# Optimization experiments

Hardware: AMD Instinct MI355X
Metric: run time of the kernel (lower is better)

## Reference

```python
import jax, jax.numpy as jnp
import numpy as np

# Criteo-like layout
B = 16384          # batch
D = 13             # num dense features
S = 26             # num sparse fields
FEAT = 100000      # one-hot depth per sparse field
K = 64             # FM latent factor dim
TOTAL = D + S * FEAT  # width of the concatenated [dense | one-hot] vector
# column offset of each sparse field's one-hot block inside the stacked vector
OFFSETS = (D + np.arange(S) * FEAT).astype(np.int32)


def setup_inputs() -> dict:
    key = jax.random.key(0)
    k1, k2, k3, k4 = jax.random.split(key, 4)
    dense_inputs = jax.random.normal(k1, (B, D), dtype=jnp.float32)
    sparse_inputs = jax.random.randint(k2, (B, S), 0, FEAT, dtype=jnp.int32)
    # FM parameters over the full stacked feature space [dense | one-hots]
    w = jax.random.normal(k3, (TOTAL, 1), dtype=jnp.float32) * 0.01  # linear weights
    V = jax.random.normal(k4, (TOTAL, K), dtype=jnp.float32) * 0.01  # factor matrix
    b = jnp.zeros((1,), dtype=jnp.float32)                           # bias w0
    return {"dense_inputs": dense_inputs, "sparse_inputs": sparse_inputs,
            "w": w, "V": V, "b": b}


def reference(dense_inputs, sparse_inputs, w, V, b):
    # Fused gather form of: one_hot(sparse) concat dense -> FM.
    # For one-hot columns, x_i is 0/1 so x @ w == gather-sum and x @ V == gather-sum.
    idx = sparse_inputs + jnp.asarray(OFFSETS)[None, :]               # [B, S] global rows
    # ---- first-order (linear) term: x @ w + b ----
    lin = dense_inputs @ w[:D] + jnp.sum(w[idx, 0], axis=1, keepdims=True) + b  # [B, 1]
    # ---- second-order FM term: 0.5 * sum_f [ (x@V)_f^2 - (x^2 @ V^2)_f ] ----
    xv = dense_inputs @ V[:D] + jnp.sum(V[idx], axis=1)               # [B, K]
    x2v2 = (dense_inputs ** 2) @ (V[:D] ** 2) + jnp.sum(V[idx] ** 2, axis=1)  # [B, K]
    inter = 0.5 * jnp.sum(xv * xv - x2v2, axis=1, keepdims=True)      # [B, 1]
    return jax.nn.sigmoid(lin + inter)
```

## Files before the change

kernel.cpp:

```cpp
#include <hip/hip_runtime.h>
#include <math.h>

#define BATCH 16384
#define DNUM  13
#define SNUM  26
#define FEAT  100000
#define KDIM  64

__global__ __launch_bounds__(256) void fm_kernel(
    const float*  __restrict__ dense,
    const int*    __restrict__ sparse,
    const float*  __restrict__ w,
    const float4* __restrict__ V4,
    const float*  __restrict__ bias,
    float*        __restrict__ out)
{
    const int wave = (blockIdx.x * blockDim.x + threadIdx.x) >> 6;
    const int lane = threadIdx.x & 63;
    if (wave >= BATCH) return;
    const int row = wave;
    const int q = lane >> 4;
    const int t = lane & 15;

    int myidx = 0;
    if (lane < SNUM) {
        myidx = sparse[row * SNUM + lane] + DNUM + lane * FEAT;
    }

    float4 xv = make_float4(0.f, 0.f, 0.f, 0.f);
    float  x2 = 0.f;
    float  lin = 0.f;

    #pragma unroll
    for (int g = 0; g < 7; ++g) {
        int s = g * 4 + q;
        if (s < SNUM) {
            int idx  = __shfl(myidx, s);
            float4 v = V4[(long long)idx * 16 + t];
            xv.x += v.x; xv.y += v.y; xv.z += v.z; xv.w += v.w;
            x2   += v.x * v.x + v.y * v.y + v.z * v.z + v.w * v.w;
        }
    }

    #pragma unroll
    for (int j = 0; j < 4; ++j) {
        int d = j * 4 + q;
        if (d < DNUM) {
            float  xd = dense[row * DNUM + d];
            float4 v  = V4[d * 16 + t];
            xv.x += xd * v.x; xv.y += xd * v.y;
            xv.z += xd * v.z; xv.w += xd * v.w;
            float xd2 = xd * xd;
            x2 += xd2 * (v.x * v.x + v.y * v.y + v.z * v.z + v.w * v.w);
        }
    }

    if (lane < SNUM) {
        lin = w[myidx];
    } else if (lane < SNUM + DNUM) {
        int d = lane - SNUM;
        lin = dense[row * DNUM + d] * w[d];
    }

    xv.x += __shfl_xor(xv.x, 16); xv.y += __shfl_xor(xv.y, 16);
    xv.z += __shfl_xor(xv.z, 16); xv.w += __shfl_xor(xv.w, 16);
    xv.x += __shfl_xor(xv.x, 32); xv.y += __shfl_xor(xv.y, 32);
    xv.z += __shfl_xor(xv.z, 32); xv.w += __shfl_xor(xv.w, 32);

    float part = 0.125f * (xv.x * xv.x + xv.y * xv.y + xv.z * xv.z + xv.w * xv.w)
               - 0.5f * x2 + lin;

    #pragma unroll
    for (int off = 32; off > 0; off >>= 1)
        part += __shfl_down(part, off);

    if (lane == 0) {
        float z = part + bias[0];
        out[row] = 1.0f / (1.0f + expf(-z));
    }
}

extern "C" void kernel_launch(void* const* d_in, const int* in_sizes, int n_in,
                              void* d_out, int out_size, void* d_ws, size_t ws_size,
                              hipStream_t stream) {
    const float*  dense  = (const float*)d_in[0];
    const int*    sparse = (const int*)d_in[1];
    const float*  w      = (const float*)d_in[2];
    const float4* V4     = (const float4*)d_in[3];
    const float*  bias   = (const float*)d_in[4];
    float* out = (float*)d_out;

    const int waves_per_block = 256 / 64;
    const int grid = (BATCH + waves_per_block - 1) / waves_per_block;
    fm_kernel<<<grid, 256, 0, stream>>>(dense, sparse, w, V4, bias, out);
}
```

Measured before the change: 739.2 us.

## Map four rows per wave with 16-lane groups and unrolled per-row gathers

Each wave now processes four batch rows, one per 16-lane group. Every group loops over all 26 sparse fields with fully unrolled float4 gathers instead of splitting fields across the four quarter-waves. This removes the cross-quarter shuffles and cuts the final reduction to 16 lanes, and it exposes 26 independent loads per thread to hide gather latency. In exchange each thread holds 26 indices in registers, and a launch-bounds occupancy hint is added. Every lane also reloads the sparse indices, which are uniform within each group.

```diff
diff --git a/kernel.cpp b/kernel.cpp
--- a/kernel.cpp
+++ b/kernel.cpp
@@ -6,8 +6,9 @@
 #define SNUM  26
 #define FEAT  100000
 #define KDIM  64
+#define RPW   4
 
-__global__ __launch_bounds__(256) void fm_kernel(
+__global__ __launch_bounds__(256, 4) void fm_kernel(
     const float*  __restrict__ dense,
     const int*    __restrict__ sparse,
     const float*  __restrict__ w,
@@ -17,64 +18,50 @@
 {
     const int wave = (blockIdx.x * blockDim.x + threadIdx.x) >> 6;
     const int lane = threadIdx.x & 63;
-    if (wave >= BATCH) return;
-    const int row = wave;
-    const int q = lane >> 4;
-    const int t = lane & 15;
+    const int g    = lane >> 4;
+    const int t    = lane & 15;
+    const int row  = wave * RPW + g;
+    const int sbase = row * SNUM;
 
-    int myidx = 0;
-    if (lane < SNUM) {
-        myidx = sparse[row * SNUM + lane] + DNUM + lane * FEAT;
-    }
+    int idx[SNUM];
+    #pragma unroll
+    for (int s = 0; s < SNUM; ++s)
+        idx[s] = sparse[sbase + s] + DNUM + s * FEAT;
+
+    float lin = w[sparse[sbase + t] + DNUM + t * FEAT];
+    if (t < SNUM - 16)
+        lin += w[sparse[sbase + t + 16] + DNUM + (t + 16) * FEAT];
+    const float* drow = dense + row * DNUM;
+    if (t < DNUM)
+        lin += drow[t] * w[t];
 
     float4 xv = make_float4(0.f, 0.f, 0.f, 0.f);
     float  x2 = 0.f;
-    float  lin = 0.f;
-
     #pragma unroll
-    for (int g = 0; g < 7; ++g) {
-        int s = g * 4 + q;
-        if (s < SNUM) {
-            int idx  = __shfl(myidx, s);
-            float4 v = V4[(long long)idx * 16 + t];
-            xv.x += v.x; xv.y += v.y; xv.z += v.z; xv.w += v.w;
-            x2   += v.x * v.x + v.y * v.y + v.z * v.z + v.w * v.w;
-        }
+    for (int s = 0; s < SNUM; ++s) {
+        float4 v = V4[idx[s] * 16 + t];
+        xv.x += v.x; xv.y += v.y; xv.z += v.z; xv.w += v.w;
+        x2   += v.x * v.x + v.y * v.y + v.z * v.z + v.w * v.w;
     }
 
     #pragma unroll
-    for (int j = 0; j < 4; ++j) {
-        int d = j * 4 + q;
-        if (d < DNUM) {
-            float  xd = dense[row * DNUM + d];
-            float4 v  = V4[d * 16 + t];
-            xv.x += xd * v.x; xv.y += xd * v.y;
-            xv.z += xd * v.z; xv.w += xd * v.w;
-            float xd2 = xd * xd;
-            x2 += xd2 * (v.x * v.x + v.y * v.y + v.z * v.z + v.w * v.w);
-        }
+    for (int d = 0; d < DNUM; ++d) {
+        float  xd = drow[d];
+        float4 v  = V4[d * 16 + t];
+        xv.x += xd * v.x; xv.y += xd * v.y;
+        xv.z += xd * v.z; xv.w += xd * v.w;
+        x2   += xd * xd * (v.x * v.x + v.y * v.y + v.z * v.z + v.w * v.w);
     }
 
-    if (lane < SNUM) {
-        lin = w[myidx];
-    } else if (lane < SNUM + DNUM) {
-        int d = lane - SNUM;
-        lin = dense[row * DNUM + d] * w[d];
-    }
+    float part = 0.5f * (xv.x * xv.x + xv.y * xv.y + xv.z * xv.z + xv.w * xv.w - x2)
+               + lin;
 
-    xv.x += __shfl_xor(xv.x, 16); xv.y += __shfl_xor(xv.y, 16);
-    xv.z += __shfl_xor(xv.z, 16); xv.w += __shfl_xor(xv.w, 16);
-    xv.x += __shfl_xor(xv.x, 32); xv.y += __shfl_xor(xv.y, 32);
-    xv.z += __shfl_xor(xv.z, 32); xv.w += __shfl_xor(xv.w, 32);
+    part += __shfl_xor(part, 1);
+    part += __shfl_xor(part, 2);
+    part += __shfl_xor(part, 4);
+    part += __shfl_xor(part, 8);
 
-    float part = 0.125f * (xv.x * xv.x + xv.y * xv.y + xv.z * xv.z + xv.w * xv.w)
-               - 0.5f * x2 + lin;
-
-    #pragma unroll
-    for (int off = 32; off > 0; off >>= 1)
-        part += __shfl_down(part, off);
-
-    if (lane == 0) {
+    if (t == 0) {
         float z = part + bias[0];
         out[row] = 1.0f / (1.0f + expf(-z));
     }
@@ -90,7 +77,7 @@
     const float*  bias   = (const float*)d_in[4];
     float* out = (float*)d_out;
 
-    const int waves_per_block = 256 / 64;
-    const int grid = (BATCH + waves_per_block - 1) / waves_per_block;
+    const int rows_per_block = (256 / 64) * RPW;
+    const int grid = BATCH / rows_per_block;
     fm_kernel<<<grid, 256, 0, stream>>>(dense, sparse, w, V4, bias, out);
 }
```

After: 735.6 us. About the same (-0.5%).
